# Performance work log

Measured on AMD Instinct MI355X. Metric: run time of the kernel, lower is better.

Reference implementation:

```python
import jax, jax.numpy as jnp
import numpy as np

IN_C = 32
OUT_C = 32
N_POLY = 3   # radial polynomial order
L_POLY = 3   # theta polynomial order
M_POLY = 3   # phi polynomial order
CONV_NUMS = 16
EPS = 1e-8


def _knn_select(pos, space_points_num, outpoint_num, conv_num):
    """Strided center sampling + KNN within each space. pos: [P,3].
    Returns global neighbor indices [space_num*outpoint_num, conv_num]."""
    P = pos.shape[0]
    S = P // space_points_num
    pos3 = pos.reshape(S, space_points_num, 3)
    stride = space_points_num // outpoint_num
    c_idx = jnp.arange(outpoint_num) * stride                       # [O]
    cpos = pos3[:, c_idx]                                           # [S,O,3]
    d2 = jnp.sum((cpos[:, :, None, :] - pos3[:, None, :, :]) ** 2, -1)  # [S,O,Ps]
    _, idx = jax.lax.top_k(-d2, conv_num)                           # [S,O,conv]
    idx = idx + (jnp.arange(S) * space_points_num)[:, None, None]
    return idx.reshape(S * outpoint_num, conv_num)


def _dcconv_forward(position_matrix, channel_matrix, coeff, bias, neighbor_indices, conv_num):
    K = neighbor_indices.shape[0]
    # --- CoordinateTransformer: gather, center, PCA rotate, spherical ---
    nbr = position_matrix[neighbor_indices]            # [K,conv,3]
    centers = nbr.mean(axis=1)                         # [K,3]
    local = nbr - centers[:, None, :]                  # [K,conv,3]
    cov = jnp.einsum('kci,kcj->kij', local, local) / conv_num
    _, V = jnp.linalg.eigh(cov)                        # [K,3,3] principal axes
    local_pca = jnp.einsum('kci,kij->kcj', local, V)   # rotate into PCA frame
    x, y, z = local_pca[..., 0], local_pca[..., 1], local_pca[..., 2]
    r = jnp.sqrt(x * x + y * y + z * z + EPS)          # [K,conv]
    theta = jnp.arccos(jnp.clip(z / r, -1.0, 1.0))
    phi = jnp.arctan2(y, x)
    # --- local features: [C_in, K, conv] (matches permute(2,0,1)) ---
    feat = channel_matrix[neighbor_indices].transpose(2, 0, 1)
    # --- DCConv3dKernelPolynomials: separable polynomial basis ---
    rp = r[..., None] ** jnp.arange(N_POLY, dtype=r.dtype)          # [K,conv,N]
    tp = theta[..., None] ** jnp.arange(L_POLY, dtype=r.dtype)      # [K,conv,L]
    pp = phi[..., None] ** jnp.arange(M_POLY, dtype=r.dtype)        # [K,conv,M]
    basis = jnp.einsum('kcn,kcl,kcm->kcnlm', rp, tp, pp)            # [K,conv,N,L,M]
    kernel_weights = jnp.einsum('kcnlm,oinlm->oikc', basis, coeff)  # [O,I,K,conv]
    # --- AggregationLayer: weighted sum over in-channels and neighbors ---
    out = jnp.einsum('ikc,oikc->ok', feat, kernel_weights)          # [O,K]
    output = out.T + bias                                           # [K,O]
    # --- resnet branch: all-ones kernel -> per-point feature sum ---
    resnet_output = jnp.broadcast_to(feat.sum(axis=(0, 2))[:, None], (K, OUT_C))
    return centers, output, resnet_output


def setup_inputs() -> dict:
    key = jax.random.key(0)
    k1, k2, k3 = jax.random.split(key, 3)
    P = 16384
    return {
        "position_matrix": jax.random.normal(k1, (P, 3), jnp.float32),
        "channel_matrix": jax.random.normal(k2, (P, IN_C), jnp.float32),
        "space_points_num": 1024,
        "outpoint_num": 256,
        "coeff": jax.random.normal(k3, (OUT_C, IN_C, N_POLY, L_POLY, M_POLY), jnp.float32) * 0.1,
        "bias": jnp.zeros((OUT_C,), jnp.float32),
    }


def reference(position_matrix, channel_matrix, space_points_num, outpoint_num, coeff, bias):
    conv_num = min(space_points_num - outpoint_num + 1, CONV_NUMS)
    neighbor_indices = _knn_select(position_matrix, space_points_num, outpoint_num, conv_num)
    return _dcconv_forward(position_matrix, channel_matrix, coeff, bias, neighbor_indices, conv_num)
```

## Files before the change

kernel.cpp:

```cpp
#include <hip/hip_runtime.h>
#include <math.h>

#define NSPACE 16
#define SPN    1024
#define OPN    256
#define STRIDE 4
#define CONV   16
#define KTOT   4096
#define INC    32
#define OUTC   32
#define NB     27
#define EPS_R  1e-8f

#define OFF_OUT 12288
#define OFF_RES 143360

#define UPDPP __builtin_amdgcn_update_dpp

__device__ __forceinline__ float wave_min64_bcast(float m) {
  int t;
  t = UPDPP(__float_as_int(m), __float_as_int(m), 0x111, 0xf, 0xf, false);
  m = fminf(m, __int_as_float(t));
  t = UPDPP(__float_as_int(m), __float_as_int(m), 0x112, 0xf, 0xf, false);
  m = fminf(m, __int_as_float(t));
  t = UPDPP(__float_as_int(m), __float_as_int(m), 0x114, 0xf, 0xf, false);
  m = fminf(m, __int_as_float(t));
  t = UPDPP(__float_as_int(m), __float_as_int(m), 0x118, 0xf, 0xf, false);
  m = fminf(m, __int_as_float(t));
  t = UPDPP(__float_as_int(m), __float_as_int(m), 0x142, 0xa, 0xf, false);
  m = fminf(m, __int_as_float(t));
  t = UPDPP(__float_as_int(m), __float_as_int(m), 0x143, 0xc, 0xf, false);
  m = fminf(m, __int_as_float(t));
  return __int_as_float(__builtin_amdgcn_readlane(__float_as_int(m), 63));
}

__device__ __forceinline__ float wave_sum64_bcast(float m) {
  int t;
  t = UPDPP(0, __float_as_int(m), 0x111, 0xf, 0xf, true); m += __int_as_float(t);
  t = UPDPP(0, __float_as_int(m), 0x112, 0xf, 0xf, true); m += __int_as_float(t);
  t = UPDPP(0, __float_as_int(m), 0x114, 0xf, 0xf, true); m += __int_as_float(t);
  t = UPDPP(0, __float_as_int(m), 0x118, 0xf, 0xf, true); m += __int_as_float(t);
  t = UPDPP(0, __float_as_int(m), 0x142, 0xa, 0xf, true); m += __int_as_float(t);
  t = UPDPP(0, __float_as_int(m), 0x143, 0xc, 0xf, true); m += __int_as_float(t);
  return __int_as_float(__builtin_amdgcn_readlane(__float_as_int(m), 63));
}

__device__ __forceinline__ float group32_sum(float m) {
  int t;
  t = UPDPP(0, __float_as_int(m), 0x111, 0xf, 0xf, true); m += __int_as_float(t);
  t = UPDPP(0, __float_as_int(m), 0x112, 0xf, 0xf, true); m += __int_as_float(t);
  t = UPDPP(0, __float_as_int(m), 0x114, 0xf, 0xf, true); m += __int_as_float(t);
  t = UPDPP(0, __float_as_int(m), 0x118, 0xf, 0xf, true); m += __int_as_float(t);
  t = UPDPP(0, __float_as_int(m), 0x142, 0xa, 0xf, true); m += __int_as_float(t);
  return m;
}


#define EIGH_Z_PARAMS                                                         \
  float &z00, float &z01, float &z02, float &z10, float &z11, float &z12,     \
  float &z20, float &z21, float &z22
#define EIGH_Z_ARGS z00, z01, z02, z10, z11, z12, z20, z21, z22

#define ROT01(c, s)                                              \
  { float _t;                                                    \
    _t = z01; z01 = (c) * _t - (s) * z00; z00 = (s) * _t + (c) * z00; \
    _t = z11; z11 = (c) * _t - (s) * z10; z10 = (s) * _t + (c) * z10; \
    _t = z21; z21 = (c) * _t - (s) * z20; z20 = (s) * _t + (c) * z20; }
#define ROT12(c, s)                                              \
  { float _t;                                                    \
    _t = z02; z02 = (c) * _t - (s) * z01; z01 = (s) * _t + (c) * z01; \
    _t = z12; z12 = (c) * _t - (s) * z11; z11 = (s) * _t + (c) * z11; \
    _t = z22; z22 = (c) * _t - (s) * z21; z21 = (s) * _t + (c) * z21; }
#define SWAP01 { float _t; _t = z00; z00 = z01; z01 = _t; _t = z10; z10 = z11; z11 = _t; _t = z20; z20 = z21; z21 = _t; }
#define SWAP02 { float _t; _t = z00; z00 = z02; z02 = _t; _t = z10; z10 = z12; z12 = _t; _t = z20; z20 = z22; z22 = _t; }
#define SWAP12 { float _t; _t = z01; z01 = z02; z02 = _t; _t = z11; z11 = z12; z12 = _t; _t = z21; z21 = z22; z22 = _t; }

__device__ __forceinline__ float f_sign(float a, float b) {
  return (b >= 0.0f) ? fabsf(a) : -fabsf(a);
}

__device__ __forceinline__ float slapy2(float x, float y) {
  float xa = fabsf(x), ya = fabsf(y);
  float w = fmaxf(xa, ya), zz = fminf(xa, ya);
  if (zz == 0.0f) return w;
  float q = zz / w;
  return w * __fsqrt_rn(1.0f + q * q);
}

__device__ __forceinline__ void slartg_(float f, float g, float* c, float* s, float* r) {
  const float safmin = 1.1754943508e-38f;
  const float safmax = 8.5070591730e+37f;
  const float rtmin  = 1.0842021725e-19f;
  const float rtmax  = 9.2233720369e+18f;
  float f1 = fabsf(f), g1 = fabsf(g);
  if (g == 0.0f) {
    *c = 1.0f; *s = 0.0f; *r = f;
  } else if (f == 0.0f) {
    *c = 0.0f; *s = (g >= 0.0f) ? 1.0f : -1.0f; *r = g1;
  } else if (f1 > rtmin && f1 < rtmax && g1 > rtmin && g1 < rtmax) {
    float d = __fsqrt_rn(f * f + g * g);
    *c = f1 / d;
    *r = (f >= 0.0f) ? d : -d;
    *s = g / (*r);
  } else {
    float u = fminf(safmax, fmaxf(safmin, fmaxf(f1, g1)));
    float fs = f / u, gs = g / u;
    float d = __fsqrt_rn(fs * fs + gs * gs);
    *c = fabsf(fs) / d;
    float rr = (f >= 0.0f) ? d : -d;
    *s = gs / rr;
    *r = rr * u;
  }
}

__device__ __forceinline__ void slaev2_(float a, float b, float c,
                                        float* rt1, float* rt2, float* cs1, float* sn1) {
  float sm = a + c;
  float df = a - c;
  float adf = fabsf(df);
  float tb = b + b;
  float ab = fabsf(tb);
  float acmx, acmn;
  if (fabsf(a) > fabsf(c)) { acmx = a; acmn = c; } else { acmx = c; acmn = a; }
  float rt;
  if (adf > ab)      { float q = ab / adf; rt = adf * __fsqrt_rn(1.0f + q * q); }
  else if (adf < ab) { float q = adf / ab; rt = ab  * __fsqrt_rn(1.0f + q * q); }
  else               { rt = ab * __fsqrt_rn(2.0f); }
  int sgn1;
  if (sm < 0.0f) {
    *rt1 = 0.5f * (sm - rt); sgn1 = -1;
    *rt2 = (acmx / *rt1) * acmn - (b / *rt1) * b;
  } else if (sm > 0.0f) {
    *rt1 = 0.5f * (sm + rt); sgn1 = 1;
    *rt2 = (acmx / *rt1) * acmn - (b / *rt1) * b;
  } else {
    *rt1 = 0.5f * rt; *rt2 = -0.5f * rt; sgn1 = 1;
  }
  float cs; int sgn2;
  if (df >= 0.0f) { cs = df + rt; sgn2 = 1; } else { cs = df - rt; sgn2 = -1; }
  float acs = fabsf(cs);
  if (acs > ab) {
    float ct = -tb / cs;
    *sn1 = 1.0f / __fsqrt_rn(1.0f + ct * ct);
    *cs1 = ct * (*sn1);
  } else {
    if (ab == 0.0f) { *cs1 = 1.0f; *sn1 = 0.0f; }
    else {
      float tn = -cs / tb;
      *cs1 = 1.0f / __fsqrt_rn(1.0f + tn * tn);
      *sn1 = tn * (*cs1);
    }
  }
  if (sgn1 == sgn2) { float tn = *cs1; *cs1 = -(*sn1); *sn1 = tn; }
}

__device__ __forceinline__ void steqr2_01(float& dA, float& eA, float& dB,
                                          bool ql, EIGH_Z_PARAMS) {
  const float eps2 = 3.5527136788e-15f, safmin = 1.1754943508e-38f;
  float tst = eA * eA;
  float thr = ql ? (eps2 * fabsf(dA)) * fabsf(dB) + safmin
                 : (eps2 * fabsf(dB)) * fabsf(dA) + safmin;
  if (tst <= thr) { eA = 0.0f; return; }
  float rt1, rt2, c, s;
  slaev2_(dA, eA, dB, &rt1, &rt2, &c, &s);
  ROT01(c, s);
  dA = rt1; dB = rt2; eA = 0.0f;
}

__device__ __forceinline__ void steqr2_12(float& dA, float& eA, float& dB,
                                          bool ql, EIGH_Z_PARAMS) {
  const float eps2 = 3.5527136788e-15f, safmin = 1.1754943508e-38f;
  float tst = eA * eA;
  float thr = ql ? (eps2 * fabsf(dA)) * fabsf(dB) + safmin
                 : (eps2 * fabsf(dB)) * fabsf(dA) + safmin;
  if (tst <= thr) { eA = 0.0f; return; }
  float rt1, rt2, c, s;
  slaev2_(dA, eA, dB, &rt1, &rt2, &c, &s);
  ROT12(c, s);
  dA = rt1; dB = rt2; eA = 0.0f;
}

__device__ __forceinline__ void steqr_ql3(float& d1, float& d2, float& d3,
                                          float& e1, float& e2, int& jtot,
                                          EIGH_Z_PARAMS) {
  const float eps2 = 3.5527136788e-15f, safmin = 1.1754943508e-38f;
  int l = 1;
  while (true) {
    if (l == 1) {
      if (e1 * e1 <= (eps2 * fabsf(d1)) * fabsf(d2) + safmin) { e1 = 0.0f; l = 2; continue; }
      if (e2 * e2 <= (eps2 * fabsf(d2)) * fabsf(d3) + safmin) {
        e2 = 0.0f;
        float rt1, rt2, c, s;
        slaev2_(d1, e1, d2, &rt1, &rt2, &c, &s);
        ROT01(c, s);
        d1 = rt1; d2 = rt2; e1 = 0.0f;
        l = 3; continue;
      }
      if (jtot == 90) return;
      jtot++;
      float p = d1;
      float g = (d2 - p) / (2.0f * e1);
      float r = slapy2(g, 1.0f);
      g = d3 - p + (e1 / (g + f_sign(r, g)));
      float s = 1.0f, c = 1.0f; p = 0.0f;
      float f, b, wc1, wc2, ws1, ws2;
      f = s * e2; b = c * e2;
      slartg_(g, f, &c, &s, &r);
      g = d3 - p;
      r = (d2 - g) * s + 2.0f * c * b;
      p = s * r;
      d3 = g + p;
      g = c * r - b;
      wc2 = c; ws2 = -s;
      f = s * e1; b = c * e1;
      slartg_(g, f, &c, &s, &r);
      e2 = r;
      g = d2 - p;
      r = (d1 - g) * s + 2.0f * c * b;
      p = s * r;
      d2 = g + p;
      g = c * r - b;
      wc1 = c; ws1 = -s;
      if (wc2 != 1.0f || ws2 != 0.0f) ROT12(wc2, ws2);
      if (wc1 != 1.0f || ws1 != 0.0f) ROT01(wc1, ws1);
      d1 = d1 - p;
      e1 = g;
      continue;
    }
    if (l == 2) {
      if (e2 * e2 <= (eps2 * fabsf(d2)) * fabsf(d3) + safmin) { e2 = 0.0f; l = 3; continue; }
      float rt1, rt2, c, s;
      slaev2_(d2, e2, d3, &rt1, &rt2, &c, &s);
      ROT12(c, s);
      d2 = rt1; d3 = rt2; e2 = 0.0f;
      return;
    }
    return;
  }
}

__device__ __forceinline__ void steqr_qr3(float& d1, float& d2, float& d3,
                                          float& e1, float& e2, int& jtot,
                                          EIGH_Z_PARAMS) {
  const float eps2 = 3.5527136788e-15f, safmin = 1.1754943508e-38f;
  int l = 3;
  while (true) {
    if (l == 3) {
      if (e2 * e2 <= (eps2 * fabsf(d3)) * fabsf(d2) + safmin) { e2 = 0.0f; l = 2; continue; }
      if (e1 * e1 <= (eps2 * fabsf(d2)) * fabsf(d1) + safmin) {
        e1 = 0.0f;
        float rt1, rt2, c, s;
        slaev2_(d2, e2, d3, &rt1, &rt2, &c, &s);
        ROT12(c, s);
        d2 = rt1; d3 = rt2; e2 = 0.0f;
        l = 1; continue;
      }
      if (jtot == 90) return;
      jtot++;
      float p = d3;
      float g = (d2 - p) / (2.0f * e2);
      float r = slapy2(g, 1.0f);
      g = d1 - p + (e2 / (g + f_sign(r, g)));
      float s = 1.0f, c = 1.0f; p = 0.0f;
      float f, b, wc1, wc2, ws1, ws2;
      f = s * e1; b = c * e1;
      slartg_(g, f, &c, &s, &r);
      g = d1 - p;
      r = (d2 - g) * s + 2.0f * c * b;
      p = s * r;
      d1 = g + p;
      g = c * r - b;
      wc1 = c; ws1 = s;
      f = s * e2; b = c * e2;
      slartg_(g, f, &c, &s, &r);
      e1 = r;
      g = d2 - p;
      r = (d3 - g) * s + 2.0f * c * b;
      p = s * r;
      d2 = g + p;
      g = c * r - b;
      wc2 = c; ws2 = s;
      if (wc1 != 1.0f || ws1 != 0.0f) ROT01(wc1, ws1);
      if (wc2 != 1.0f || ws2 != 0.0f) ROT12(wc2, ws2);
      d3 = d3 - p;
      e2 = g;
      continue;
    }
    if (l == 2) {
      if (e1 * e1 <= (eps2 * fabsf(d2)) * fabsf(d1) + safmin) { e1 = 0.0f; l = 1; continue; }
      float rt1, rt2, c, s;
      slaev2_(d1, e1, d2, &rt1, &rt2, &c, &s);
      ROT01(c, s);
      d1 = rt1; d2 = rt2; e1 = 0.0f;
      return;
    }
    return;
  }
}

__device__ __forceinline__ void ssteqr3s(float& d1, float& d2, float& d3,
                                         float& e1, float& e2, EIGH_Z_PARAMS) {
  const float eps    = 5.9604644775e-08f;
  const float ssfmax = 3.0744573457e+18f;
  const float ssfmin = 3.0517578125e-05f;
  int jtot = 0;
  int m;
  {
    float tst = fabsf(e1);
    if (tst == 0.0f) m = 1;
    else if (tst <= (__fsqrt_rn(fabsf(d1)) * __fsqrt_rn(fabsf(d2))) * eps) { e1 = 0.0f; m = 1; }
    else {
      tst = fabsf(e2);
      if (tst == 0.0f) m = 2;
      else if (tst <= (__fsqrt_rn(fabsf(d2)) * __fsqrt_rn(fabsf(d3))) * eps) { e2 = 0.0f; m = 2; }
      else m = 3;
    }
  }
  if (m == 3) {
    float anorm = fmaxf(fmaxf(fabsf(d1), fabsf(d2)), fabsf(d3));
    anorm = fmaxf(anorm, fmaxf(fabsf(e1), fabsf(e2)));
    if (anorm != 0.0f) {
      int iscale = 0; float mul;
      if (anorm > ssfmax) {
        iscale = 1; mul = ssfmax / anorm;
        d1 *= mul; d2 *= mul; d3 *= mul; e1 *= mul; e2 *= mul;
      } else if (anorm < ssfmin) {
        iscale = 2; mul = ssfmin / anorm;
        d1 *= mul; d2 *= mul; d3 *= mul; e1 *= mul; e2 *= mul;
      }
      if (fabsf(d3) < fabsf(d1)) steqr_qr3(d1, d2, d3, e1, e2, jtot, EIGH_Z_ARGS);
      else                       steqr_ql3(d1, d2, d3, e1, e2, jtot, EIGH_Z_ARGS);
      if (iscale == 1) {
        mul = anorm / ssfmax;
        d1 *= mul; d2 *= mul; d3 *= mul; e1 *= mul; e2 *= mul;
      } else if (iscale == 2) {
        mul = anorm / ssfmin;
        d1 *= mul; d2 *= mul; d3 *= mul; e1 *= mul; e2 *= mul;
      }
    }
  } else if (m == 2) {
    float anorm = fmaxf(fmaxf(fabsf(d1), fabsf(d2)), fabsf(e1));
    if (anorm != 0.0f) {
      int iscale = 0; float mul;
      if (anorm > ssfmax) { iscale = 1; mul = ssfmax / anorm; d1 *= mul; d2 *= mul; e1 *= mul; }
      else if (anorm < ssfmin) { iscale = 2; mul = ssfmin / anorm; d1 *= mul; d2 *= mul; e1 *= mul; }
      steqr2_01(d1, e1, d2, !(fabsf(d2) < fabsf(d1)), EIGH_Z_ARGS);
      if (iscale == 1) { mul = anorm / ssfmax; d1 *= mul; d2 *= mul; e1 *= mul; }
      else if (iscale == 2) { mul = anorm / ssfmin; d1 *= mul; d2 *= mul; e1 *= mul; }
    }
  } else {
    int m2;
    float tst = fabsf(e2);
    if (tst == 0.0f) m2 = 2;
    else if (tst <= (__fsqrt_rn(fabsf(d2)) * __fsqrt_rn(fabsf(d3))) * eps) { e2 = 0.0f; m2 = 2; }
    else m2 = 3;
    if (m2 == 3) {
      float anorm = fmaxf(fmaxf(fabsf(d2), fabsf(d3)), fabsf(e2));
      if (anorm != 0.0f) {
        int iscale = 0; float mul;
        if (anorm > ssfmax) { iscale = 1; mul = ssfmax / anorm; d2 *= mul; d3 *= mul; e2 *= mul; }
        else if (anorm < ssfmin) { iscale = 2; mul = ssfmin / anorm; d2 *= mul; d3 *= mul; e2 *= mul; }
        steqr2_12(d2, e2, d3, !(fabsf(d3) < fabsf(d2)), EIGH_Z_ARGS);
        if (iscale == 1) { mul = anorm / ssfmax; d2 *= mul; d3 *= mul; e2 *= mul; }
        else if (iscale == 2) { mul = anorm / ssfmin; d2 *= mul; d3 *= mul; e2 *= mul; }
      }
    }
  }
  {
    int k = 1; float p = d1;
    if (d2 < p) { k = 2; p = d2; }
    if (d3 < p) { k = 3; p = d3; }
    if (k == 2)      { d2 = d1; d1 = p; SWAP01; }
    else if (k == 3) { d3 = d1; d1 = p; SWAP02; }
    if (d3 < d2) { p = d3; d3 = d2; d2 = p; SWAP12; }
  }
}

__device__ __forceinline__ void eigh3(float a11, float a21, float a31,
                                      float a22, float a32, float a33,
                                      EIGH_Z_PARAMS) {
  float tau1 = 0.0f, v3 = 0.0f, e1;
  float xnorm = fabsf(a31);
  if (xnorm == 0.0f) {
    tau1 = 0.0f;
    e1 = a21;
    v3 = 0.0f;
  } else {
    float beta = -f_sign(slapy2(a21, xnorm), a21);
    tau1 = (beta - a21) / beta;
    v3 = a31 / (a21 - beta);
    e1 = beta;
  }
  if (tau1 != 0.0f) {
    float x1 = tau1 * (a22 + a32 * v3);
    float x2 = tau1 * (a32 + a33 * v3);
    float alpha = -0.5f * tau1 * (x1 + x2 * v3);
    float w1 = x1 + alpha;
    float w2 = x2 + alpha * v3;
    a22 = a22 - w1 - w1;
    a32 = a32 - v3 * w1 - w2;
    a33 = a33 - v3 * w2 - w2 * v3;
  }
  float d1 = a11, d2 = a22, d3 = a33, e2 = a32;
  z00 = 1.0f; z01 = 0.0f; z02 = 0.0f;
  z10 = 0.0f; z11 = 1.0f; z12 = 0.0f;
  z20 = 0.0f; z21 = 0.0f; z22 = 1.0f;
  ssteqr3s(d1, d2, d3, e1, e2, EIGH_Z_ARGS);
  if (tau1 != 0.0f) {
    float tt;
    tt = z10 + v3 * z20; z10 -= tau1 * tt; z20 -= tau1 * tt * v3;
    tt = z11 + v3 * z21; z11 -= tau1 * tt; z21 -= tau1 * tt * v3;
    tt = z12 + v3 * z22; z12 -= tau1 * tt; z22 -= tau1 * tt * v3;
  }
}


#define CE(i, j)                                                  \
  {                                                               \
    unsigned long long ta = K[i], tb = K[j];                      \
    bool sw = tb < ta;                                            \
    K[i] = sw ? tb : ta;                                          \
    K[j] = sw ? ta : tb;                                          \
  }

#define RFL(x) __int_as_float(__builtin_amdgcn_readfirstlane(__float_as_int(x)))

__global__ __launch_bounds__(256, 2) void dcconv_fused(
    const float* __restrict__ pos, const float* __restrict__ chan,
    const float* __restrict__ coeff, const float* __restrict__ bias,
    float* __restrict__ out) {
  const int t    = threadIdx.x;
  const int wv   = t >> 6;
  const int lane = t & 63;
  const int kglob = blockIdx.x * 4 + wv;
  const int sp   = kglob >> 8;
  const int ci   = kglob & 255;
  const int base = sp * SPN;

  __shared__ __align__(16) float basis_sh[4][CONV][28];
  __shared__ __align__(16) float feat_sh[4][CONV][INC];
  __shared__ __align__(16) float G_sh[4][INC][28];

  const int cgl = base + ci * STRIDE;
  const float cx = pos[cgl * 3 + 0];
  const float cy = pos[cgl * 3 + 1];
  const float cz = pos[cgl * 3 + 2];

  unsigned long long K[16];
#pragma unroll
  for (int u = 0; u < 16; ++u) {
    const int j = u * 64 + lane;
    const float px = pos[(base + j) * 3 + 0];
    const float py = pos[(base + j) * 3 + 1];
    const float pz = pos[(base + j) * 3 + 2];
    float dx = __fsub_rn(cx, px), dy = __fsub_rn(cy, py), dz = __fsub_rn(cz, pz);
    float d2 = __fadd_rn(__fadd_rn(__fmul_rn(dx, dx), __fmul_rn(dy, dy)),
                         __fmul_rn(dz, dz));
    K[u] = (((unsigned long long)__float_as_uint(d2)) << 32) | (unsigned)j;
  }

  CE(0, 1) CE(2, 3) CE(4, 5) CE(6, 7) CE(8, 9) CE(10, 11) CE(12, 13) CE(14, 15)
  CE(0, 2) CE(1, 3) CE(4, 6) CE(5, 7) CE(8, 10) CE(9, 11) CE(12, 14) CE(13, 15)
  CE(1, 2) CE(5, 6) CE(9, 10) CE(13, 14)
  CE(0, 4) CE(1, 5) CE(2, 6) CE(3, 7) CE(8, 12) CE(9, 13) CE(10, 14) CE(11, 15)
  CE(2, 4) CE(3, 5) CE(10, 12) CE(11, 13)
  CE(1, 2) CE(3, 4) CE(5, 6) CE(9, 10) CE(11, 12) CE(13, 14)
  CE(0, 8) CE(1, 9) CE(2, 10) CE(3, 11) CE(4, 12) CE(5, 13) CE(6, 14) CE(7, 15)
  CE(4, 8) CE(5, 9) CE(6, 10) CE(7, 11)
  CE(2, 4) CE(3, 5) CE(6, 8) CE(7, 9) CE(10, 12) CE(11, 13)
  CE(1, 2) CE(3, 4) CE(5, 6) CE(7, 8) CE(9, 10) CE(11, 12) CE(13, 14)

  int myidx = cgl;
#pragma unroll 1
  for (int it = 0; it < CONV; ++it) {
    const float f0 = __uint_as_float((unsigned)(K[0] >> 32));
    const float m = wave_min64_bcast(f0);
    const unsigned long long msk = __ballot(f0 == m);
    const int wl = (int)__builtin_ctzll(msk);
    const int widx = __builtin_amdgcn_readlane((int)(unsigned)(K[0] & 0xffffffffu), wl);
    if (lane == it) myidx = base + widx;
    const bool on = (lane == wl);
#pragma unroll
    for (int u = 0; u < 15; ++u) K[u] = on ? K[u + 1] : K[u];
    K[15] = on ? ~0ull : K[15];
  }

  float nx = 0.0f, ny = 0.0f, nz = 0.0f;
  if (lane < CONV) {
    const float* pp = pos + myidx * 3;
    nx = pp[0]; ny = pp[1]; nz = pp[2];
  }

  const float mx = wave_sum64_bcast(nx) * 0.0625f;
  const float my = wave_sum64_bcast(ny) * 0.0625f;
  const float mz = wave_sum64_bcast(nz) * 0.0625f;
  if (lane == 0) {
    out[kglob * 3 + 0] = mx; out[kglob * 3 + 1] = my; out[kglob * 3 + 2] = mz;
  }
  const float lx = nx - mx, ly = ny - my, lz = nz - mz;
  const float lxm = (lane < CONV) ? lx : 0.0f;
  const float lym = (lane < CONV) ? ly : 0.0f;
  const float lzm = (lane < CONV) ? lz : 0.0f;
  const float inv = 1.0f / (float)CONV;
  const float c00 = wave_sum64_bcast(lxm * lxm) * inv;
  const float c10 = wave_sum64_bcast(lym * lxm) * inv;
  const float c20 = wave_sum64_bcast(lzm * lxm) * inv;
  const float c11 = wave_sum64_bcast(lym * lym) * inv;
  const float c21 = wave_sum64_bcast(lzm * lym) * inv;
  const float c22 = wave_sum64_bcast(lzm * lzm) * inv;

  float V00 = 0, V01 = 0, V02 = 0, V10 = 0, V11 = 0, V12 = 0,
        V20 = 0, V21 = 0, V22 = 0;
  if (lane == 0) {
    eigh3(c00, c10, c20, c11, c21, c22,
          V00, V01, V02, V10, V11, V12, V20, V21, V22);
  }
  V00 = RFL(V00); V01 = RFL(V01); V02 = RFL(V02);
  V10 = RFL(V10); V11 = RFL(V11); V12 = RFL(V12);
  V20 = RFL(V20); V21 = RFL(V21); V22 = RFL(V22);

  const int hc = lane >> 5;
  const int ifeat = lane & 31;
  float fv0, fv1, fv2, fv3, fv4, fv5, fv6, fv7;
  {
    int g;
    g = __shfl(myidx,  0 + hc); fv0 = chan[g * INC + ifeat];
    g = __shfl(myidx,  2 + hc); fv1 = chan[g * INC + ifeat];
    g = __shfl(myidx,  4 + hc); fv2 = chan[g * INC + ifeat];
    g = __shfl(myidx,  6 + hc); fv3 = chan[g * INC + ifeat];
    g = __shfl(myidx,  8 + hc); fv4 = chan[g * INC + ifeat];
    g = __shfl(myidx, 10 + hc); fv5 = chan[g * INC + ifeat];
    g = __shfl(myidx, 12 + hc); fv6 = chan[g * INC + ifeat];
    g = __shfl(myidx, 14 + hc); fv7 = chan[g * INC + ifeat];
  }

  if (lane < CONV) {
    float x = lx * V00 + ly * V10 + lz * V20;
    float y = lx * V01 + ly * V11 + lz * V21;
    float z = lx * V02 + ly * V12 + lz * V22;
    float r = __fsqrt_rn(x * x + y * y + z * z + EPS_R);
    float ct = fminf(fmaxf(z / r, -1.0f), 1.0f);
    float theta = acosf(ct);
    float phi = atan2f(y, x);
    const float r1 = r, r2 = r * r;
    const float t1 = theta, t2 = theta * theta;
    const float p1 = phi, p2 = phi * phi;
    float4* bp = (float4*)(&basis_sh[wv][lane][0]);
    bp[0] = make_float4(1.0f,      p1,        p2,        t1);
    bp[1] = make_float4(t1 * p1,   t1 * p2,   t2,        t2 * p1);
    bp[2] = make_float4(t2 * p2,   r1,        r1 * p1,   r1 * p2);
    bp[3] = make_float4(r1 * t1,   r1 * t1 * p1, r1 * t1 * p2, r1 * t2);
    bp[4] = make_float4(r1 * t2 * p1, r1 * t2 * p2, r2,  r2 * p1);
    bp[5] = make_float4(r2 * p2,   r2 * t1,   r2 * t1 * p1, r2 * t1 * p2);
    bp[6] = make_float4(r2 * t2,   r2 * t2 * p1, r2 * t2 * p2, 0.0f);
  }

  feat_sh[wv][ 0 + hc][ifeat] = fv0;
  feat_sh[wv][ 2 + hc][ifeat] = fv1;
  feat_sh[wv][ 4 + hc][ifeat] = fv2;
  feat_sh[wv][ 6 + hc][ifeat] = fv3;
  feat_sh[wv][ 8 + hc][ifeat] = fv4;
  feat_sh[wv][10 + hc][ifeat] = fv5;
  feat_sh[wv][12 + hc][ifeat] = fv6;
  feat_sh[wv][14 + hc][ifeat] = fv7;
  float s_loc = ((fv0 + fv1) + (fv2 + fv3)) + ((fv4 + fv5) + (fv6 + fv7));
  const float sres = wave_sum64_bcast(s_loc);
  if (lane < OUTC) out[OFF_RES + kglob * OUTC + lane] = sres;

  {
    const int gi = lane >> 1;
    const int jh = lane & 1;
    const int jr0 = jh ? 12 : 0;
    float a[16];
#pragma unroll
    for (int jj = 0; jj < 16; ++jj) a[jj] = 0.0f;
#pragma unroll
    for (int c = 0; c < CONV; ++c) {
      const float f = feat_sh[wv][c][gi];
      const float4* bp = (const float4*)(&basis_sh[wv][c][jr0]);
#pragma unroll
      for (int q = 0; q < 4; ++q) {
        const float4 v4 = bp[q];
        a[4 * q + 0] += f * v4.x; a[4 * q + 1] += f * v4.y;
        a[4 * q + 2] += f * v4.z; a[4 * q + 3] += f * v4.w;
      }
    }
    if (jh == 0) {
      float4* gp = (float4*)(&G_sh[wv][gi][0]);
      gp[0] = make_float4(a[0], a[1], a[2], a[3]);
      gp[1] = make_float4(a[4], a[5], a[6], a[7]);
      gp[2] = make_float4(a[8], a[9], a[10], a[11]);
      gp[3] = make_float4(a[12], a[13], a[14], a[15]);
    } else {
      float4* gp = (float4*)(&G_sh[wv][gi][16]);
      gp[0] = make_float4(a[4], a[5], a[6], a[7]);
      gp[1] = make_float4(a[8], a[9], a[10], a[11]);
      gp[2] = make_float4(a[12], a[13], a[14], a[15]);
    }
  }

  __syncthreads();

  {
    const int ir = t & 31;
    const int oh = t >> 5;
    const int l32 = lane & 31;
#pragma unroll
    for (int p = 0; p < 2; ++p) {
      const int o0 = oh * 4 + p * 2;
      float cf0[27], cf1[27];
      const float* cA = coeff + (o0 * INC + ir) * NB;
      const float* cB = coeff + ((o0 + 1) * INC + ir) * NB;
#pragma unroll
      for (int jj = 0; jj < 27; ++jj) { cf0[jj] = cA[jj]; cf1[jj] = cB[jj]; }
      float s0c0 = 0, s0c1 = 0, s0c2 = 0, s0c3 = 0;
      float s1c0 = 0, s1c1 = 0, s1c2 = 0, s1c3 = 0;
#pragma unroll
      for (int cc = 0; cc < 4; ++cc) {
        float gr[28];
        const float4* gp = (const float4*)(&G_sh[cc][ir][0]);
#pragma unroll
        for (int q = 0; q < 7; ++q) {
          const float4 v4 = gp[q];
          gr[q * 4 + 0] = v4.x; gr[q * 4 + 1] = v4.y;
          gr[q * 4 + 2] = v4.z; gr[q * 4 + 3] = v4.w;
        }
        float s0 = 0.0f, s1 = 0.0f;
#pragma unroll
        for (int jj = 0; jj < 27; ++jj) {
          s0 += gr[jj] * cf0[jj];
          s1 += gr[jj] * cf1[jj];
        }
        if (cc == 0) { s0c0 = s0; s1c0 = s1; }
        else if (cc == 1) { s0c1 = s0; s1c1 = s1; }
        else if (cc == 2) { s0c2 = s0; s1c2 = s1; }
        else { s0c3 = s0; s1c3 = s1; }
      }
      s0c0 = group32_sum(s0c0); s0c1 = group32_sum(s0c1);
      s0c2 = group32_sum(s0c2); s0c3 = group32_sum(s0c3);
      s1c0 = group32_sum(s1c0); s1c1 = group32_sum(s1c1);
      s1c2 = group32_sum(s1c2); s1c3 = group32_sum(s1c3);
      if (l32 == 31) {
        const float b0 = bias[o0], b1 = bias[o0 + 1];
        const int kb = blockIdx.x * 4;
        out[OFF_OUT + (kb + 0) * OUTC + o0] = s0c0 + b0;
        out[OFF_OUT + (kb + 1) * OUTC + o0] = s0c1 + b0;
        out[OFF_OUT + (kb + 2) * OUTC + o0] = s0c2 + b0;
        out[OFF_OUT + (kb + 3) * OUTC + o0] = s0c3 + b0;
        out[OFF_OUT + (kb + 0) * OUTC + o0 + 1] = s1c0 + b1;
        out[OFF_OUT + (kb + 1) * OUTC + o0 + 1] = s1c1 + b1;
        out[OFF_OUT + (kb + 2) * OUTC + o0 + 1] = s1c2 + b1;
        out[OFF_OUT + (kb + 3) * OUTC + o0 + 1] = s1c3 + b1;
      }
    }
  }
}

extern "C" void kernel_launch(void* const* d_in, const int* in_sizes, int n_in,
                              void* d_out, int out_size, void* d_ws, size_t ws_size,
                              hipStream_t stream) {
  const float* pos   = (const float*)d_in[0];
  const float* chan  = (const float*)d_in[1];
  const float* coeff = (const float*)d_in[4];
  const float* bias  = (const float*)d_in[5];
  float* out = (float*)d_out;
  dcconv_fused<<<dim3(KTOT / 4), dim3(256), 0, stream>>>(pos, chan, coeff, bias, out);
}
```

Measured before the change: 34.85 us.

## Split KNN search across two waves per center with bitonic merge of candidates

Each output center is now handled by a pair of waves: each wave scans half of the 1024 space points, keeps its local top-16 in registers, and writes the candidates to shared memory. A 32-lane bitonic merge then picks the final 16 neighbours. The block grows to 512 threads, feature gathering and the residual sum are split across the two waves, and the coefficient contraction is spread over twice as many threads. This is meant to halve the serial per-wave selection and sorting cost and raise parallelism, at the price of extra barriers, shared-memory traffic and a second wave that sits idle during the PCA and basis stage.

```diff
diff --git a/kernel.cpp b/kernel.cpp
--- a/kernel.cpp
+++ b/kernel.cpp
@@ -425,14 +425,16 @@
 
 #define RFL(x) __int_as_float(__builtin_amdgcn_readfirstlane(__float_as_int(x)))
 
-__global__ __launch_bounds__(256, 2) void dcconv_fused(
+__global__ __launch_bounds__(512, 8) void dcconv_fused(
     const float* __restrict__ pos, const float* __restrict__ chan,
     const float* __restrict__ coeff, const float* __restrict__ bias,
     float* __restrict__ out) {
   const int t    = threadIdx.x;
   const int wv   = t >> 6;
+  const int pair = wv >> 1;
+  const int h    = wv & 1;
   const int lane = t & 63;
-  const int kglob = blockIdx.x * 4 + wv;
+  const int kglob = blockIdx.x * 4 + pair;
   const int sp   = kglob >> 8;
   const int ci   = kglob & 255;
   const int base = sp * SPN;
@@ -440,16 +442,18 @@
   __shared__ __align__(16) float basis_sh[4][CONV][28];
   __shared__ __align__(16) float feat_sh[4][CONV][INC];
   __shared__ __align__(16) float G_sh[4][INC][28];
+  __shared__ unsigned long long cand_sh[4][2][CONV];
+  __shared__ float res_sh[4][2];
 
   const int cgl = base + ci * STRIDE;
   const float cx = pos[cgl * 3 + 0];
   const float cy = pos[cgl * 3 + 1];
   const float cz = pos[cgl * 3 + 2];
 
-  unsigned long long K[16];
-#pragma unroll
-  for (int u = 0; u < 16; ++u) {
-    const int j = u * 64 + lane;
+  unsigned long long K[8];
+#pragma unroll
+  for (int u = 0; u < 8; ++u) {
+    const int j = h * 512 + u * 64 + lane;
     const float px = pos[(base + j) * 3 + 0];
     const float py = pos[(base + j) * 3 + 1];
     const float pz = pos[(base + j) * 3 + 2];
@@ -459,115 +463,131 @@
     K[u] = (((unsigned long long)__float_as_uint(d2)) << 32) | (unsigned)j;
   }
 
-  CE(0, 1) CE(2, 3) CE(4, 5) CE(6, 7) CE(8, 9) CE(10, 11) CE(12, 13) CE(14, 15)
-  CE(0, 2) CE(1, 3) CE(4, 6) CE(5, 7) CE(8, 10) CE(9, 11) CE(12, 14) CE(13, 15)
-  CE(1, 2) CE(5, 6) CE(9, 10) CE(13, 14)
-  CE(0, 4) CE(1, 5) CE(2, 6) CE(3, 7) CE(8, 12) CE(9, 13) CE(10, 14) CE(11, 15)
-  CE(2, 4) CE(3, 5) CE(10, 12) CE(11, 13)
-  CE(1, 2) CE(3, 4) CE(5, 6) CE(9, 10) CE(11, 12) CE(13, 14)
-  CE(0, 8) CE(1, 9) CE(2, 10) CE(3, 11) CE(4, 12) CE(5, 13) CE(6, 14) CE(7, 15)
-  CE(4, 8) CE(5, 9) CE(6, 10) CE(7, 11)
-  CE(2, 4) CE(3, 5) CE(6, 8) CE(7, 9) CE(10, 12) CE(11, 13)
-  CE(1, 2) CE(3, 4) CE(5, 6) CE(7, 8) CE(9, 10) CE(11, 12) CE(13, 14)
-
-  int myidx = cgl;
+  CE(0, 1) CE(2, 3) CE(4, 5) CE(6, 7)
+  CE(0, 2) CE(1, 3) CE(4, 6) CE(5, 7)
+  CE(1, 2) CE(5, 6)
+  CE(0, 4) CE(1, 5) CE(2, 6) CE(3, 7)
+  CE(2, 4) CE(3, 5)
+  CE(1, 2) CE(3, 4) CE(5, 6)
+
+  unsigned long long ck = ~0ull;
 #pragma unroll 1
   for (int it = 0; it < CONV; ++it) {
     const float f0 = __uint_as_float((unsigned)(K[0] >> 32));
     const float m = wave_min64_bcast(f0);
     const unsigned long long msk = __ballot(f0 == m);
     const int wl = (int)__builtin_ctzll(msk);
-    const int widx = __builtin_amdgcn_readlane((int)(unsigned)(K[0] & 0xffffffffu), wl);
-    if (lane == it) myidx = base + widx;
+    const unsigned lo =
+        (unsigned)__builtin_amdgcn_readlane((int)(unsigned)(K[0] & 0xffffffffu), wl);
+    if (lane == it)
+      ck = (((unsigned long long)__float_as_uint(m)) << 32) | lo;
     const bool on = (lane == wl);
 #pragma unroll
-    for (int u = 0; u < 15; ++u) K[u] = on ? K[u + 1] : K[u];
-    K[15] = on ? ~0ull : K[15];
-  }
-
-  float nx = 0.0f, ny = 0.0f, nz = 0.0f;
-  if (lane < CONV) {
-    const float* pp = pos + myidx * 3;
-    nx = pp[0]; ny = pp[1]; nz = pp[2];
-  }
-
-  const float mx = wave_sum64_bcast(nx) * 0.0625f;
-  const float my = wave_sum64_bcast(ny) * 0.0625f;
-  const float mz = wave_sum64_bcast(nz) * 0.0625f;
-  if (lane == 0) {
-    out[kglob * 3 + 0] = mx; out[kglob * 3 + 1] = my; out[kglob * 3 + 2] = mz;
-  }
-  const float lx = nx - mx, ly = ny - my, lz = nz - mz;
-  const float lxm = (lane < CONV) ? lx : 0.0f;
-  const float lym = (lane < CONV) ? ly : 0.0f;
-  const float lzm = (lane < CONV) ? lz : 0.0f;
-  const float inv = 1.0f / (float)CONV;
-  const float c00 = wave_sum64_bcast(lxm * lxm) * inv;
-  const float c10 = wave_sum64_bcast(lym * lxm) * inv;
-  const float c20 = wave_sum64_bcast(lzm * lxm) * inv;
-  const float c11 = wave_sum64_bcast(lym * lym) * inv;
-  const float c21 = wave_sum64_bcast(lzm * lym) * inv;
-  const float c22 = wave_sum64_bcast(lzm * lzm) * inv;
-
-  float V00 = 0, V01 = 0, V02 = 0, V10 = 0, V11 = 0, V12 = 0,
-        V20 = 0, V21 = 0, V22 = 0;
-  if (lane == 0) {
-    eigh3(c00, c10, c20, c11, c21, c22,
-          V00, V01, V02, V10, V11, V12, V20, V21, V22);
-  }
-  V00 = RFL(V00); V01 = RFL(V01); V02 = RFL(V02);
-  V10 = RFL(V10); V11 = RFL(V11); V12 = RFL(V12);
-  V20 = RFL(V20); V21 = RFL(V21); V22 = RFL(V22);
+    for (int u = 0; u < 7; ++u) K[u] = on ? K[u + 1] : K[u];
+    K[7] = on ? ~0ull : K[7];
+  }
+  if (lane < CONV) cand_sh[pair][h][lane] = ck;
+
+  __syncthreads();
+
+  unsigned long long km = ~0ull;
+  if (lane < 16)      km = cand_sh[pair][0][lane];
+  else if (lane < 32) km = cand_sh[pair][1][31 - lane];
+#pragma unroll
+  for (int d = 16; d >= 1; d >>= 1) {
+    unsigned long long o = __shfl_xor(km, d);
+    const bool up = ((lane & d) == 0);
+    const unsigned long long mn = (km < o) ? km : o;
+    const unsigned long long mx = (km < o) ? o : km;
+    km = up ? mn : mx;
+  }
+  int myidx = base;
+  if (lane < CONV) myidx = base + (int)(unsigned)(km & 0xffffffffu);
 
   const int hc = lane >> 5;
   const int ifeat = lane & 31;
-  float fv0, fv1, fv2, fv3, fv4, fv5, fv6, fv7;
+  float fv0, fv1, fv2, fv3;
   {
+    const int cb = h * 8 + hc;
     int g;
-    g = __shfl(myidx,  0 + hc); fv0 = chan[g * INC + ifeat];
-    g = __shfl(myidx,  2 + hc); fv1 = chan[g * INC + ifeat];
-    g = __shfl(myidx,  4 + hc); fv2 = chan[g * INC + ifeat];
-    g = __shfl(myidx,  6 + hc); fv3 = chan[g * INC + ifeat];
-    g = __shfl(myidx,  8 + hc); fv4 = chan[g * INC + ifeat];
-    g = __shfl(myidx, 10 + hc); fv5 = chan[g * INC + ifeat];
-    g = __shfl(myidx, 12 + hc); fv6 = chan[g * INC + ifeat];
-    g = __shfl(myidx, 14 + hc); fv7 = chan[g * INC + ifeat];
-  }
-
-  if (lane < CONV) {
-    float x = lx * V00 + ly * V10 + lz * V20;
-    float y = lx * V01 + ly * V11 + lz * V21;
-    float z = lx * V02 + ly * V12 + lz * V22;
-    float r = __fsqrt_rn(x * x + y * y + z * z + EPS_R);
-    float ct = fminf(fmaxf(z / r, -1.0f), 1.0f);
-    float theta = acosf(ct);
-    float phi = atan2f(y, x);
-    const float r1 = r, r2 = r * r;
-    const float t1 = theta, t2 = theta * theta;
-    const float p1 = phi, p2 = phi * phi;
-    float4* bp = (float4*)(&basis_sh[wv][lane][0]);
-    bp[0] = make_float4(1.0f,      p1,        p2,        t1);
-    bp[1] = make_float4(t1 * p1,   t1 * p2,   t2,        t2 * p1);
-    bp[2] = make_float4(t2 * p2,   r1,        r1 * p1,   r1 * p2);
-    bp[3] = make_float4(r1 * t1,   r1 * t1 * p1, r1 * t1 * p2, r1 * t2);
-    bp[4] = make_float4(r1 * t2 * p1, r1 * t2 * p2, r2,  r2 * p1);
-    bp[5] = make_float4(r2 * p2,   r2 * t1,   r2 * t1 * p1, r2 * t1 * p2);
-    bp[6] = make_float4(r2 * t2,   r2 * t2 * p1, r2 * t2 * p2, 0.0f);
-  }
-
-  feat_sh[wv][ 0 + hc][ifeat] = fv0;
-  feat_sh[wv][ 2 + hc][ifeat] = fv1;
-  feat_sh[wv][ 4 + hc][ifeat] = fv2;
-  feat_sh[wv][ 6 + hc][ifeat] = fv3;
-  feat_sh[wv][ 8 + hc][ifeat] = fv4;
-  feat_sh[wv][10 + hc][ifeat] = fv5;
-  feat_sh[wv][12 + hc][ifeat] = fv6;
-  feat_sh[wv][14 + hc][ifeat] = fv7;
-  float s_loc = ((fv0 + fv1) + (fv2 + fv3)) + ((fv4 + fv5) + (fv6 + fv7));
-  const float sres = wave_sum64_bcast(s_loc);
-  if (lane < OUTC) out[OFF_RES + kglob * OUTC + lane] = sres;
+    g = __shfl(myidx, cb + 0); fv0 = chan[g * INC + ifeat];
+    g = __shfl(myidx, cb + 2); fv1 = chan[g * INC + ifeat];
+    g = __shfl(myidx, cb + 4); fv2 = chan[g * INC + ifeat];
+    g = __shfl(myidx, cb + 6); fv3 = chan[g * INC + ifeat];
+  }
+
+  if (h == 0) {
+    float nx = 0.0f, ny = 0.0f, nz = 0.0f;
+    if (lane < CONV) {
+      const float* pp = pos + myidx * 3;
+      nx = pp[0]; ny = pp[1]; nz = pp[2];
+    }
+    const float mx = wave_sum64_bcast(nx) * 0.0625f;
+    const float my = wave_sum64_bcast(ny) * 0.0625f;
+    const float mz = wave_sum64_bcast(nz) * 0.0625f;
+    if (lane == 0) {
+      out[kglob * 3 + 0] = mx; out[kglob * 3 + 1] = my; out[kglob * 3 + 2] = mz;
+    }
+    const float lx = nx - mx, ly = ny - my, lz = nz - mz;
+    const float lxm = (lane < CONV) ? lx : 0.0f;
+    const float lym = (lane < CONV) ? ly : 0.0f;
+    const float lzm = (lane < CONV) ? lz : 0.0f;
+    const float inv = 1.0f / (float)CONV;
+    const float c00 = wave_sum64_bcast(lxm * lxm) * inv;
+    const float c10 = wave_sum64_bcast(lym * lxm) * inv;
+    const float c20 = wave_sum64_bcast(lzm * lxm) * inv;
+    const float c11 = wave_sum64_bcast(lym * lym) * inv;
+    const float c21 = wave_sum64_bcast(lzm * lym) * inv;
+    const float c22 = wave_sum64_bcast(lzm * lzm) * inv;
+
+    float V00 = 0, V01 = 0, V02 = 0, V10 = 0, V11 = 0, V12 = 0,
+          V20 = 0, V21 = 0, V22 = 0;
+    if (lane == 0) {
+      eigh3(c00, c10, c20, c11, c21, c22,
+            V00, V01, V02, V10, V11, V12, V20, V21, V22);
+    }
+    V00 = RFL(V00); V01 = RFL(V01); V02 = RFL(V02);
+    V10 = RFL(V10); V11 = RFL(V11); V12 = RFL(V12);
+    V20 = RFL(V20); V21 = RFL(V21); V22 = RFL(V22);
+
+    if (lane < CONV) {
+      float x = lx * V00 + ly * V10 + lz * V20;
+      float y = lx * V01 + ly * V11 + lz * V21;
+      float z = lx * V02 + ly * V12 + lz * V22;
+      float r = __fsqrt_rn(x * x + y * y + z * z + EPS_R);
+      float ct = fminf(fmaxf(z / r, -1.0f), 1.0f);
+      float theta = acosf(ct);
+      float phi = atan2f(y, x);
+      const float r1 = r, r2 = r * r;
+      const float t1 = theta, t2 = theta * theta;
+      const float p1 = phi, p2 = phi * phi;
+      float4* bp = (float4*)(&basis_sh[pair][lane][0]);
+      bp[0] = make_float4(1.0f,      p1,        p2,        t1);
+      bp[1] = make_float4(t1 * p1,   t1 * p2,   t2,        t2 * p1);
+      bp[2] = make_float4(t2 * p2,   r1,        r1 * p1,   r1 * p2);
+      bp[3] = make_float4(r1 * t1,   r1 * t1 * p1, r1 * t1 * p2, r1 * t2);
+      bp[4] = make_float4(r1 * t2 * p1, r1 * t2 * p2, r2,  r2 * p1);
+      bp[5] = make_float4(r2 * p2,   r2 * t1,   r2 * t1 * p1, r2 * t1 * p2);
+      bp[6] = make_float4(r2 * t2,   r2 * t2 * p1, r2 * t2 * p2, 0.0f);
+    }
+  }
 
   {
+    const int cb = h * 8 + hc;
+    feat_sh[pair][cb + 0][ifeat] = fv0;
+    feat_sh[pair][cb + 2][ifeat] = fv1;
+    feat_sh[pair][cb + 4][ifeat] = fv2;
+    feat_sh[pair][cb + 6][ifeat] = fv3;
+  }
+  {
+    float s_loc = (fv0 + fv1) + (fv2 + fv3);
+    const float sres = wave_sum64_bcast(s_loc);
+    if (lane == 0) res_sh[pair][h] = sres;
+  }
+
+  __syncthreads();
+
+  if (h == 0) {
     const int gi = lane >> 1;
     const int jh = lane & 1;
     const int jr0 = jh ? 12 : 0;
@@ -576,8 +596,8 @@
     for (int jj = 0; jj < 16; ++jj) a[jj] = 0.0f;
 #pragma unroll
     for (int c = 0; c < CONV; ++c) {
-      const float f = feat_sh[wv][c][gi];
-      const float4* bp = (const float4*)(&basis_sh[wv][c][jr0]);
+      const float f = feat_sh[pair][c][gi];
+      const float4* bp = (const float4*)(&basis_sh[pair][c][jr0]);
 #pragma unroll
       for (int q = 0; q < 4; ++q) {
         const float4 v4 = bp[q];
@@ -586,17 +606,20 @@
       }
     }
     if (jh == 0) {
-      float4* gp = (float4*)(&G_sh[wv][gi][0]);
+      float4* gp = (float4*)(&G_sh[pair][gi][0]);
       gp[0] = make_float4(a[0], a[1], a[2], a[3]);
       gp[1] = make_float4(a[4], a[5], a[6], a[7]);
       gp[2] = make_float4(a[8], a[9], a[10], a[11]);
       gp[3] = make_float4(a[12], a[13], a[14], a[15]);
     } else {
-      float4* gp = (float4*)(&G_sh[wv][gi][16]);
+      float4* gp = (float4*)(&G_sh[pair][gi][16]);
       gp[0] = make_float4(a[4], a[5], a[6], a[7]);
       gp[1] = make_float4(a[8], a[9], a[10], a[11]);
       gp[2] = make_float4(a[12], a[13], a[14], a[15]);
     }
+  } else {
+    if (lane < OUTC)
+      out[OFF_RES + kglob * OUTC + lane] = res_sh[pair][0] + res_sh[pair][1];
   }
 
   __syncthreads();
@@ -605,53 +628,50 @@
     const int ir = t & 31;
     const int oh = t >> 5;
     const int l32 = lane & 31;
-#pragma unroll
-    for (int p = 0; p < 2; ++p) {
-      const int o0 = oh * 4 + p * 2;
-      float cf0[27], cf1[27];
-      const float* cA = coeff + (o0 * INC + ir) * NB;
-      const float* cB = coeff + ((o0 + 1) * INC + ir) * NB;
-#pragma unroll
-      for (int jj = 0; jj < 27; ++jj) { cf0[jj] = cA[jj]; cf1[jj] = cB[jj]; }
-      float s0c0 = 0, s0c1 = 0, s0c2 = 0, s0c3 = 0;
-      float s1c0 = 0, s1c1 = 0, s1c2 = 0, s1c3 = 0;
-#pragma unroll
-      for (int cc = 0; cc < 4; ++cc) {
-        float gr[28];
-        const float4* gp = (const float4*)(&G_sh[cc][ir][0]);
-#pragma unroll
-        for (int q = 0; q < 7; ++q) {
-          const float4 v4 = gp[q];
-          gr[q * 4 + 0] = v4.x; gr[q * 4 + 1] = v4.y;
-          gr[q * 4 + 2] = v4.z; gr[q * 4 + 3] = v4.w;
-        }
-        float s0 = 0.0f, s1 = 0.0f;
-#pragma unroll
-        for (int jj = 0; jj < 27; ++jj) {
-          s0 += gr[jj] * cf0[jj];
-          s1 += gr[jj] * cf1[jj];
-        }
-        if (cc == 0) { s0c0 = s0; s1c0 = s1; }
-        else if (cc == 1) { s0c1 = s0; s1c1 = s1; }
-        else if (cc == 2) { s0c2 = s0; s1c2 = s1; }
-        else { s0c3 = s0; s1c3 = s1; }
-      }
-      s0c0 = group32_sum(s0c0); s0c1 = group32_sum(s0c1);
-      s0c2 = group32_sum(s0c2); s0c3 = group32_sum(s0c3);
-      s1c0 = group32_sum(s1c0); s1c1 = group32_sum(s1c1);
-      s1c2 = group32_sum(s1c2); s1c3 = group32_sum(s1c3);
-      if (l32 == 31) {
-        const float b0 = bias[o0], b1 = bias[o0 + 1];
-        const int kb = blockIdx.x * 4;
-        out[OFF_OUT + (kb + 0) * OUTC + o0] = s0c0 + b0;
-        out[OFF_OUT + (kb + 1) * OUTC + o0] = s0c1 + b0;
-        out[OFF_OUT + (kb + 2) * OUTC + o0] = s0c2 + b0;
-        out[OFF_OUT + (kb + 3) * OUTC + o0] = s0c3 + b0;
-        out[OFF_OUT + (kb + 0) * OUTC + o0 + 1] = s1c0 + b1;
-        out[OFF_OUT + (kb + 1) * OUTC + o0 + 1] = s1c1 + b1;
-        out[OFF_OUT + (kb + 2) * OUTC + o0 + 1] = s1c2 + b1;
-        out[OFF_OUT + (kb + 3) * OUTC + o0 + 1] = s1c3 + b1;
-      }
+    const int o0 = oh * 2;
+    float cf0[27], cf1[27];
+    const float* cA = coeff + (o0 * INC + ir) * NB;
+    const float* cB = coeff + ((o0 + 1) * INC + ir) * NB;
+#pragma unroll
+    for (int jj = 0; jj < 27; ++jj) { cf0[jj] = cA[jj]; cf1[jj] = cB[jj]; }
+    float s0c0 = 0, s0c1 = 0, s0c2 = 0, s0c3 = 0;
+    float s1c0 = 0, s1c1 = 0, s1c2 = 0, s1c3 = 0;
+#pragma unroll
+    for (int cc = 0; cc < 4; ++cc) {
+      float gr[28];
+      const float4* gp = (const float4*)(&G_sh[cc][ir][0]);
+#pragma unroll
+      for (int q = 0; q < 7; ++q) {
+        const float4 v4 = gp[q];
+        gr[q * 4 + 0] = v4.x; gr[q * 4 + 1] = v4.y;
+        gr[q * 4 + 2] = v4.z; gr[q * 4 + 3] = v4.w;
+      }
+      float s0 = 0.0f, s1 = 0.0f;
+#pragma unroll
+      for (int jj = 0; jj < 27; ++jj) {
+        s0 += gr[jj] * cf0[jj];
+        s1 += gr[jj] * cf1[jj];
+      }
+      if (cc == 0) { s0c0 = s0; s1c0 = s1; }
+      else if (cc == 1) { s0c1 = s0; s1c1 = s1; }
+      else if (cc == 2) { s0c2 = s0; s1c2 = s1; }
+      else { s0c3 = s0; s1c3 = s1; }
+    }
+    s0c0 = group32_sum(s0c0); s0c1 = group32_sum(s0c1);
+    s0c2 = group32_sum(s0c2); s0c3 = group32_sum(s0c3);
+    s1c0 = group32_sum(s1c0); s1c1 = group32_sum(s1c1);
+    s1c2 = group32_sum(s1c2); s1c3 = group32_sum(s1c3);
+    if (l32 == 31) {
+      const float b0 = bias[o0], b1 = bias[o0 + 1];
+      const int kb = blockIdx.x * 4;
+      out[OFF_OUT + (kb + 0) * OUTC + o0] = s0c0 + b0;
+      out[OFF_OUT + (kb + 1) * OUTC + o0] = s0c1 + b0;
+      out[OFF_OUT + (kb + 2) * OUTC + o0] = s0c2 + b0;
+      out[OFF_OUT + (kb + 3) * OUTC + o0] = s0c3 + b0;
+      out[OFF_OUT + (kb + 0) * OUTC + o0 + 1] = s1c0 + b1;
+      out[OFF_OUT + (kb + 1) * OUTC + o0 + 1] = s1c1 + b1;
+      out[OFF_OUT + (kb + 2) * OUTC + o0 + 1] = s1c2 + b1;
+      out[OFF_OUT + (kb + 3) * OUTC + o0 + 1] = s1c3 + b1;
     }
   }
 }
@@ -664,5 +684,5 @@
   const float* coeff = (const float*)d_in[4];
   const float* bias  = (const float*)d_in[5];
   float* out = (float*)d_out;
-  dcconv_fused<<<dim3(KTOT / 4), dim3(256), 0, stream>>>(pos, chan, coeff, bias, out);
-}
+  dcconv_fused<<<dim3(KTOT / 4), dim3(512), 0, stream>>>(pos, chan, coeff, bias, out);
+}
```

Result: slower. 46.03 us (+32.1%).
